# Kernel tuning notes

Measured on AMD Instinct MI355X. Metric: run time of the kernel, lower is better.

## Reference

```python
import jax, jax.numpy as jnp
import numpy as np

N_SRC = 50000      # columns of adj / rows of x
N_SAMP = 50000     # rows of adj (sampled nodes this layer)
N_TOTAL = 200000   # rows of historical embedding buffer
E = 1600000        # nnz of adj
D_IN = 256
D_OUT = 256


def setup_inputs() -> dict:
    key = jax.random.key(0)
    ks = jax.random.split(key, 10)
    x = jax.random.normal(ks[0], (N_SRC, D_IN), dtype=jnp.float32)
    adj_row = jax.random.randint(ks[1], (E,), 0, N_SAMP, dtype=jnp.int32)
    adj_col = jax.random.randint(ks[2], (E,), 0, N_SRC, dtype=jnp.int32)
    adj_val = jax.random.uniform(ks[3], (E,), dtype=jnp.float32)
    nodes_per_layer = jax.random.randint(ks[4], (N_SAMP,), 0, N_TOTAL, dtype=jnp.int32)
    y_buf = jax.random.normal(ks[5], (N_TOTAL, D_IN), dtype=jnp.float32)
    W = jax.random.normal(ks[6], (D_IN, D_OUT), dtype=jnp.float32) / np.sqrt(D_IN)
    b = jax.random.normal(ks[7], (D_OUT,), dtype=jnp.float32) * 0.01
    scale = jnp.ones((D_OUT,), dtype=jnp.float32)
    offset = jnp.zeros((D_OUT,), dtype=jnp.float32)
    return {"x": x, "adj_row": adj_row, "adj_col": adj_col, "adj_val": adj_val,
            "nodes_per_layer": nodes_per_layer, "y_buf": y_buf,
            "W": W, "b": b, "scale": scale, "offset": offset}


def reference(x, adj_row, adj_col, adj_val, nodes_per_layer, y_buf, W, b, scale, offset):
    # ---- sparse aggregation: feat = spmm(adj, x)  [N_SAMP, D_IN]
    msgs = adj_val[:, None] * x[adj_col]                         # [E, D_IN]
    feat = jax.ops.segment_sum(msgs, adj_row, num_segments=N_SAMP)
    # ---- momentum blend with historical embeddings (training path)
    feat = 0.9 * y_buf[nodes_per_layer] + 0.1 * feat
    # buffer update: sampled rows <- feat.detach(); all other rows *= 0.9
    new_y = (y_buf * 0.9).at[nodes_per_layer].set(jax.lax.stop_gradient(feat))
    # ---- linear -> ELU -> custom per-row normalization
    out = jax.nn.elu(feat @ W + b)                               # [N_SAMP, D_OUT]
    mean = out.mean(axis=1, keepdims=True)
    var = out.var(axis=1, keepdims=True) + 1e-9                  # unbiased=False
    out = (out - mean) * scale * jax.lax.rsqrt(var) + offset
    return out, new_y
```

## Files before the change

kernel.cpp:

```cpp
#include <hip/hip_runtime.h>
#include <hip/hip_fp16.h>
#include <math.h>

#define N_SRC   50000
#define N_SAMP  50000
#define N_TOTAL 200000
#define NE      1600000
#define D       256

#define CBSHIFT 11
#define NB      25
#define NCELL   (N_SAMP * NB)

typedef unsigned short ushort;
typedef unsigned int   uint;
using bf16x8 = __attribute__((ext_vector_type(8))) short;
using f32x4v = __attribute__((ext_vector_type(4))) float;

__device__ __forceinline__ float4 ntload4(const float* p) {
    f32x4v t = __builtin_nontemporal_load((const f32x4v*)p);
    return make_float4(t.x, t.y, t.z, t.w);
}
__device__ __forceinline__ void ntstore4(float* p, float4 v) {
    f32x4v t; t.x = v.x; t.y = v.y; t.z = v.z; t.w = v.w;
    __builtin_nontemporal_store(t, (f32x4v*)p);
}

__device__ __forceinline__ ushort bf16_rne(float f) {
    uint u = __float_as_uint(f);
    uint r = u + 0x7FFFu + ((u >> 16) & 1u);
    return (ushort)(r >> 16);
}
__device__ __forceinline__ float bf16_tof(ushort h) {
    return __uint_as_float(((uint)h) << 16);
}

__device__ __forceinline__ float4 xload4h(const __half* p) {
    int2 r = *(const int2*)p;
    __half2 h0 = *(__half2*)&r.x;
    __half2 h1 = *(__half2*)&r.y;
    float2 f0 = __half22float2(h0);
    float2 f1 = __half22float2(h1);
    return make_float4(f0.x, f0.y, f1.x, f1.y);
}

__device__ __forceinline__ void eunpack(uint e, int& col, float& val) {
    col = (int)(e & 0xFFFFu);
    val = __half2float(__ushort_as_half((ushort)(e >> 16)));
}

__global__ __launch_bounds__(256) void k_setup(
    int* __restrict__ cellcnt, int* __restrict__ owner, int* __restrict__ gtotal,
    const float* __restrict__ x, __half* __restrict__ xh,
    const float* __restrict__ W, ushort* __restrict__ Wt_hi, ushort* __restrict__ Wt_lo)
{
    int i = blockIdx.x * 256 + threadIdx.x;
    if (i < NCELL)   cellcnt[i] = 0;
    if (i < N_TOTAL) owner[i]   = -1;
    if (i == 0)      *gtotal    = 0;
    if (i < (N_SRC * D) / 8) {
        float4 a = ntload4(x + (size_t)i * 8);
        float4 c = ntload4(x + (size_t)i * 8 + 4);
        __half2 h0 = __floats2half2_rn(a.x, a.y);
        __half2 h1 = __floats2half2_rn(a.z, a.w);
        __half2 h2 = __floats2half2_rn(c.x, c.y);
        __half2 h3 = __floats2half2_rn(c.z, c.w);
        int4 w;
        w.x = *(int*)&h0; w.y = *(int*)&h1; w.z = *(int*)&h2; w.w = *(int*)&h3;
        *(int4*)(xh + (size_t)i * 8) = w;
    }
    if (i < D * D) {
        int k = i >> 8;
        int n = i & 255;
        float f = W[i];
        ushort h = bf16_rne(f);
        ushort l = bf16_rne(f - bf16_tof(h));
        Wt_hi[n * D + k] = h;
        Wt_lo[n * D + k] = l;
    }
}

__global__ __launch_bounds__(256) void k_count(
    const int* __restrict__ adj_row, const int* __restrict__ adj_col,
    const int* __restrict__ nodes, int* __restrict__ cellcnt, int* __restrict__ owner)
{
    int idx = blockIdx.x * 256 + threadIdx.x;
    if (idx < NE) {
        int row = __builtin_nontemporal_load(adj_row + idx);
        int col = __builtin_nontemporal_load(adj_col + idx);
        atomicAdd(&cellcnt[row * NB + (col >> CBSHIFT)], 1);
    }
    if (idx < N_SAMP) {
        atomicMax(&owner[nodes[idx]], idx);
    }
}

__global__ __launch_bounds__(256) void k_rowalloc(
    const int* __restrict__ cellcnt, int* __restrict__ cellcur,
    int* __restrict__ rowptr, int* __restrict__ rowcnt, int* __restrict__ gtotal)
{
    int r = blockIdx.x * 256 + threadIdx.x;
    if (r >= N_SAMP) return;
    int pref[NB];
    int sum = 0;
    #pragma unroll
    for (int cb = 0; cb < NB; ++cb) {
        pref[cb] = sum;
        sum += cellcnt[r * NB + cb];
    }
    int base = atomicAdd(gtotal, (sum + 3) & ~3);
    rowptr[r] = base;
    rowcnt[r] = sum;
    #pragma unroll
    for (int cb = 0; cb < NB; ++cb)
        cellcur[r * NB + cb] = base + pref[cb];
}

__global__ __launch_bounds__(256) void k_scatter(
    const int* __restrict__ adj_row, const int* __restrict__ adj_col,
    const float* __restrict__ adj_val, int* __restrict__ cellcur, uint* __restrict__ bucket)
{
    int idx = blockIdx.x * 256 + threadIdx.x;
    if (idx >= NE) return;
    int   row = __builtin_nontemporal_load(adj_row + idx);
    int   col = __builtin_nontemporal_load(adj_col + idx);
    float val = __builtin_nontemporal_load(adj_val + idx);
    uint  e   = (uint)col | ((uint)__half_as_ushort(__float2half_rn(val)) << 16);
    int pos = atomicAdd(&cellcur[row * NB + (col >> CBSHIFT)], 1);
    bucket[pos] = e;
}

__global__ __launch_bounds__(256) void k_spmm_blend(
    const __half* __restrict__ xh, const uint* __restrict__ bucket,
    const int* __restrict__ rowptr, const int* __restrict__ rowcnt,
    const int* __restrict__ nodes, const int* __restrict__ owner,
    const float* __restrict__ y_buf, float* __restrict__ feat, float* __restrict__ newy)
{
    int wave = threadIdx.x >> 6;
    int lane = threadIdx.x & 63;
    int row  = blockIdx.x * 4 + wave;
    int off  = lane * 4;

    int cnt = rowcnt[row];
    const uint* bk = bucket + rowptr[row];
    float4 acc = make_float4(0.f, 0.f, 0.f, 0.f);
    int j = 0;
    for (; j + 3 < cnt; j += 4) {
        uint4 ev = *(const uint4*)(bk + j);
        int c0, c1, c2, c3; float v0, v1, v2, v3;
        eunpack(ev.x, c0, v0); eunpack(ev.y, c1, v1);
        eunpack(ev.z, c2, v2); eunpack(ev.w, c3, v3);
        float4 x0 = xload4h(xh + (size_t)c0 * D + off);
        float4 x1 = xload4h(xh + (size_t)c1 * D + off);
        float4 x2 = xload4h(xh + (size_t)c2 * D + off);
        float4 x3 = xload4h(xh + (size_t)c3 * D + off);
        acc.x += v0 * x0.x + v1 * x1.x + v2 * x2.x + v3 * x3.x;
        acc.y += v0 * x0.y + v1 * x1.y + v2 * x2.y + v3 * x3.y;
        acc.z += v0 * x0.z + v1 * x1.z + v2 * x2.z + v3 * x3.z;
        acc.w += v0 * x0.w + v1 * x1.w + v2 * x2.w + v3 * x3.w;
    }
    for (; j < cnt; ++j) {
        int c0; float v0;
        eunpack(bk[j], c0, v0);
        float4 x0 = xload4h(xh + (size_t)c0 * D + off);
        acc.x += v0 * x0.x; acc.y += v0 * x0.y;
        acc.z += v0 * x0.z; acc.w += v0 * x0.w;
    }
    int node = nodes[row];
    float4 yv = *(const float4*)(y_buf + (size_t)node * D + off);
    float4 f;
    f.x = 0.9f * yv.x + 0.1f * acc.x;
    f.y = 0.9f * yv.y + 0.1f * acc.y;
    f.z = 0.9f * yv.z + 0.1f * acc.z;
    f.w = 0.9f * yv.w + 0.1f * acc.w;
    *(float4*)(feat + (size_t)row * D + off) = f;
    if (owner[node] == row)
        ntstore4(newy + (size_t)node * D + off, f);

    int base = row * 4;
    int4 ow = *(const int4*)&owner[base];
    #pragma unroll
    for (int k = 0; k < 4; ++k) {
        int o = (k == 0) ? ow.x : (k == 1) ? ow.y : (k == 2) ? ow.z : ow.w;
        if (o < 0) {
            int r = base + k;
            float4 y = *(const float4*)(y_buf + (size_t)r * D + off);
            ntstore4(newy + (size_t)r * D + off,
                     make_float4(0.9f * y.x, 0.9f * y.y, 0.9f * y.z, 0.9f * y.w));
        }
    }
}

__global__ __launch_bounds__(256) void k_gemm_elu_norm(
    float* __restrict__ io, const ushort* __restrict__ Wt_hi,
    const ushort* __restrict__ Wt_lo, const float* __restrict__ b,
    const float* __restrict__ scale, const float* __restrict__ offset)
{
    __shared__ ushort Fhi[32][264], Flo[32][264];
    __shared__ ushort Wh[256][40],  Wl[256][40];
    __shared__ float  red[2][2][16][2];

    int tid  = threadIdx.x;
    int w    = tid >> 6;
    int l    = tid & 63;
    int g    = l >> 4;
    int c16  = l & 15;
    int mt   = w & 1;
    int nh   = w >> 1;
    int r0   = blockIdx.x * 32;

    {
        int m  = tid >> 3;
        int c0 = (tid & 7) * 32;
        int r  = r0 + m;
        #pragma unroll
        for (int i = 0; i < 8; ++i) {
            float4 v = (r < N_SAMP) ? *(const float4*)(io + (size_t)r * D + c0 + i * 4)
                                    : make_float4(0.f, 0.f, 0.f, 0.f);
            ushort h0 = bf16_rne(v.x), h1 = bf16_rne(v.y);
            ushort h2 = bf16_rne(v.z), h3 = bf16_rne(v.w);
            ushort l0 = bf16_rne(v.x - bf16_tof(h0));
            ushort l1 = bf16_rne(v.y - bf16_tof(h1));
            ushort l2 = bf16_rne(v.z - bf16_tof(h2));
            ushort l3 = bf16_rne(v.w - bf16_tof(h3));
            int c = c0 + i * 4;
            uint2 ph, pl;
            ph.x = (uint)h0 | ((uint)h1 << 16); ph.y = (uint)h2 | ((uint)h3 << 16);
            pl.x = (uint)l0 | ((uint)l1 << 16); pl.y = (uint)l2 | ((uint)l3 << 16);
            *(uint2*)&Fhi[m][c] = ph;
            *(uint2*)&Flo[m][c] = pl;
        }
    }

    f32x4v acc[8];
    #pragma unroll
    for (int t = 0; t < 8; ++t) acc[t] = (f32x4v)(0.f);

    for (int kt8 = 0; kt8 < 8; ++kt8) {
        int kt = kt8 * 32;
        __syncthreads();
        {
            int n = tid;
            const int4* gh = (const int4*)(Wt_hi + (size_t)n * D + kt);
            const int4* gl = (const int4*)(Wt_lo + (size_t)n * D + kt);
            #pragma unroll
            for (int i = 0; i < 4; ++i) {
                *(int4*)&Wh[n][i * 8] = gh[i];
                *(int4*)&Wl[n][i * 8] = gl[i];
            }
        }
        __syncthreads();
        int arow = mt * 16 + c16;
        bf16x8 ah = *(const bf16x8*)&Fhi[arow][kt + g * 8];
        bf16x8 al = *(const bf16x8*)&Flo[arow][kt + g * 8];
        #pragma unroll
        for (int t = 0; t < 8; ++t) {
            int n = nh * 128 + t * 16 + c16;
            bf16x8 bh = *(const bf16x8*)&Wh[n][g * 8];
            bf16x8 bl = *(const bf16x8*)&Wl[n][g * 8];
            acc[t] = __builtin_amdgcn_mfma_f32_16x16x32_bf16(ah, bh, acc[t], 0, 0, 0);
            acc[t] = __builtin_amdgcn_mfma_f32_16x16x32_bf16(al, bh, acc[t], 0, 0, 0);
            acc[t] = __builtin_amdgcn_mfma_f32_16x16x32_bf16(ah, bl, acc[t], 0, 0, 0);
        }
    }

    float bcol[8], scol[8], ocol[8];
    #pragma unroll
    for (int t = 0; t < 8; ++t) {
        int c = nh * 128 + t * 16 + c16;
        bcol[t] = b[c]; scol[t] = scale[c]; ocol[t] = offset[c];
    }
    float s[4] = {0.f, 0.f, 0.f, 0.f};
    float q[4] = {0.f, 0.f, 0.f, 0.f};
    #pragma unroll
    for (int t = 0; t < 8; ++t) {
        #pragma unroll
        for (int j = 0; j < 4; ++j) {
            float o = acc[t][j] + bcol[t];
            o = o > 0.f ? o : expf(o) - 1.f;
            acc[t][j] = o;
            s[j] += o;
            q[j] += o * o;
        }
    }
    #pragma unroll
    for (int j = 0; j < 4; ++j) {
        #pragma unroll
        for (int d2 = 1; d2 < 16; d2 <<= 1) {
            s[j] += __shfl_xor(s[j], d2, 64);
            q[j] += __shfl_xor(q[j], d2, 64);
        }
    }
    if (c16 == 0) {
        #pragma unroll
        for (int j = 0; j < 4; ++j) {
            red[mt][nh][g * 4 + j][0] = s[j];
            red[mt][nh][g * 4 + j][1] = q[j];
        }
    }
    __syncthreads();
    #pragma unroll
    for (int j = 0; j < 4; ++j) {
        int rr = g * 4 + j;
        float S = red[mt][0][rr][0] + red[mt][1][rr][0];
        float Q = red[mt][0][rr][1] + red[mt][1][rr][1];
        float mean = S * (1.0f / 256.0f);
        float var  = Q * (1.0f / 256.0f) - mean * mean + 1e-9f;
        float rstd = rsqrtf(var);
        int r = r0 + mt * 16 + rr;
        if (r < N_SAMP) {
            #pragma unroll
            for (int t = 0; t < 8; ++t) {
                int c = nh * 128 + t * 16 + c16;
                io[(size_t)r * D + c] = (acc[t][j] - mean) * scol[t] * rstd + ocol[t];
            }
        }
    }
}

extern "C" void kernel_launch(void* const* d_in, const int* in_sizes, int n_in,
                              void* d_out, int out_size, void* d_ws, size_t ws_size,
                              hipStream_t stream) {
    const float* x       = (const float*)d_in[0];
    const int*   adj_row = (const int*)  d_in[1];
    const int*   adj_col = (const int*)  d_in[2];
    const float* adj_val = (const float*)d_in[3];
    const int*   nodes   = (const int*)  d_in[4];
    const float* y_buf   = (const float*)d_in[5];
    const float* Wm      = (const float*)d_in[6];
    const float* b       = (const float*)d_in[7];
    const float* scale   = (const float*)d_in[8];
    const float* offset  = (const float*)d_in[9];

    float* out  = (float*)d_out;
    float* newy = out + (size_t)N_SAMP * D;

    char*   ws      = (char*)d_ws;
    int*    cellcnt = (int*)(ws);
    int*    cellcur = (int*)(ws + 5  * 1024 * 1024);
    int*    rowptr  = (int*)(ws + 10 * 1024 * 1024);
    int*    rowcnt  = (int*)(ws + 10 * 1024 * 1024 + 256 * 1024);
    int*    gtotal  = (int*)(ws + 10 * 1024 * 1024 + 512 * 1024);
    int*    owner   = (int*)(ws + 11 * 1024 * 1024);
    ushort* Wt_hi   = (ushort*)(ws + 12 * 1024 * 1024);
    ushort* Wt_lo   = (ushort*)(ws + 12 * 1024 * 1024 + 128 * 1024);
    uint*   bucket  = (uint*)(ws + 13 * 1024 * 1024);
    __half* xh      = (__half*)(ws + 20 * 1024 * 1024);

    int setup_threads = (N_SRC * D) / 8;
    k_setup   <<<(setup_threads + 255) / 256, 256, 0, stream>>>(
        cellcnt, owner, gtotal, x, xh, Wm, Wt_hi, Wt_lo);
    k_count   <<<(NE + 255) / 256,     256, 0, stream>>>(adj_row, adj_col, nodes, cellcnt, owner);
    k_rowalloc<<<(N_SAMP + 255) / 256, 256, 0, stream>>>(cellcnt, cellcur, rowptr, rowcnt, gtotal);
    k_scatter <<<(NE + 255) / 256,     256, 0, stream>>>(adj_row, adj_col, adj_val, cellcur, bucket);
    k_spmm_blend<<<N_SAMP / 4, 256, 0, stream>>>(
        xh, bucket, rowptr, rowcnt, nodes, owner, y_buf, out, newy);
    k_gemm_elu_norm<<<(N_SAMP + 31) / 32, 256, 0, stream>>>(out, Wt_hi, Wt_lo, b, scale, offset);
}
```

Before: 786.9 us.

## Fuse CSR build kernels into one cooperative kernel, widen spmm unroll, coarser column buckets

Merges the setup, count, row-alloc and scatter kernels into one cooperative kernel with grid-wide syncs, which removes three launches and the gaps between them. Column buckets become coarser (13 instead of 25 per row), which shrinks the cell arrays. The SpMM inner loop is unrolled to 8 gathers per iteration to keep more loads in flight, and y_buf reads become nontemporal. The costs are grid-sync overhead, a fixed 1024-block grid that must be co-resident, and more register pressure in the SpMM loop.

```diff
diff --git a/kernel.cpp b/kernel.cpp
--- a/kernel.cpp
+++ b/kernel.cpp
@@ -1,6 +1,9 @@
 #include <hip/hip_runtime.h>
 #include <hip/hip_fp16.h>
+#include <hip/hip_cooperative_groups.h>
 #include <math.h>
+
+namespace cg = cooperative_groups;
 
 #define N_SRC   50000
 #define N_SAMP  50000
@@ -8,8 +11,8 @@
 #define NE      1600000
 #define D       256
 
-#define CBSHIFT 11
-#define NB      25
+#define CBSHIFT 12
+#define NB      13
 #define NCELL   (N_SAMP * NB)
 
 typedef unsigned short ushort;
@@ -49,16 +52,23 @@
     val = __half2float(__ushort_as_half((ushort)(e >> 16)));
 }
 
-__global__ __launch_bounds__(256) void k_setup(
-    int* __restrict__ cellcnt, int* __restrict__ owner, int* __restrict__ gtotal,
+__global__ __launch_bounds__(256, 4) void k_build(
     const float* __restrict__ x, __half* __restrict__ xh,
-    const float* __restrict__ W, ushort* __restrict__ Wt_hi, ushort* __restrict__ Wt_lo)
+    const float* __restrict__ W, ushort* __restrict__ Wt_hi, ushort* __restrict__ Wt_lo,
+    const int* __restrict__ adj_row, const int* __restrict__ adj_col,
+    const float* __restrict__ adj_val, const int* __restrict__ nodes,
+    int* __restrict__ cellcnt, int* __restrict__ cellcur,
+    int* __restrict__ rowptr, int* __restrict__ rowcnt,
+    int* __restrict__ gtotal, int* __restrict__ owner, uint* __restrict__ bucket)
 {
-    int i = blockIdx.x * 256 + threadIdx.x;
-    if (i < NCELL)   cellcnt[i] = 0;
-    if (i < N_TOTAL) owner[i]   = -1;
-    if (i == 0)      *gtotal    = 0;
-    if (i < (N_SRC * D) / 8) {
+    cg::grid_group grid = cg::this_grid();
+    int tid = blockIdx.x * 256 + threadIdx.x;
+    int nth = gridDim.x * 256;
+
+    for (int i = tid; i < NCELL; i += nth) cellcnt[i] = 0;
+    for (int i = tid; i < N_TOTAL; i += nth) owner[i] = -1;
+    if (tid == 0) *gtotal = 0;
+    for (int i = tid; i < (N_SRC * D) / 8; i += nth) {
         float4 a = ntload4(x + (size_t)i * 8);
         float4 c = ntload4(x + (size_t)i * 8 + 4);
         __half2 h0 = __floats2half2_rn(a.x, a.y);
@@ -69,7 +79,7 @@
         w.x = *(int*)&h0; w.y = *(int*)&h1; w.z = *(int*)&h2; w.w = *(int*)&h3;
         *(int4*)(xh + (size_t)i * 8) = w;
     }
-    if (i < D * D) {
+    for (int i = tid; i < D * D; i += nth) {
         int k = i >> 8;
         int n = i & 255;
         float f = W[i];
@@ -78,56 +88,43 @@
         Wt_hi[n * D + k] = h;
         Wt_lo[n * D + k] = l;
     }
-}
-
-__global__ __launch_bounds__(256) void k_count(
-    const int* __restrict__ adj_row, const int* __restrict__ adj_col,
-    const int* __restrict__ nodes, int* __restrict__ cellcnt, int* __restrict__ owner)
-{
-    int idx = blockIdx.x * 256 + threadIdx.x;
-    if (idx < NE) {
-        int row = __builtin_nontemporal_load(adj_row + idx);
-        int col = __builtin_nontemporal_load(adj_col + idx);
+    grid.sync();
+
+    for (int i = tid; i < NE; i += nth) {
+        int row = __builtin_nontemporal_load(adj_row + i);
+        int col = __builtin_nontemporal_load(adj_col + i);
         atomicAdd(&cellcnt[row * NB + (col >> CBSHIFT)], 1);
     }
-    if (idx < N_SAMP) {
-        atomicMax(&owner[nodes[idx]], idx);
-    }
-}
-
-__global__ __launch_bounds__(256) void k_rowalloc(
-    const int* __restrict__ cellcnt, int* __restrict__ cellcur,
-    int* __restrict__ rowptr, int* __restrict__ rowcnt, int* __restrict__ gtotal)
-{
-    int r = blockIdx.x * 256 + threadIdx.x;
-    if (r >= N_SAMP) return;
-    int pref[NB];
-    int sum = 0;
-    #pragma unroll
-    for (int cb = 0; cb < NB; ++cb) {
-        pref[cb] = sum;
-        sum += cellcnt[r * NB + cb];
-    }
-    int base = atomicAdd(gtotal, (sum + 3) & ~3);
-    rowptr[r] = base;
-    rowcnt[r] = sum;
-    #pragma unroll
-    for (int cb = 0; cb < NB; ++cb)
-        cellcur[r * NB + cb] = base + pref[cb];
-}
-
-__global__ __launch_bounds__(256) void k_scatter(
-    const int* __restrict__ adj_row, const int* __restrict__ adj_col,
-    const float* __restrict__ adj_val, int* __restrict__ cellcur, uint* __restrict__ bucket)
-{
-    int idx = blockIdx.x * 256 + threadIdx.x;
-    if (idx >= NE) return;
-    int   row = __builtin_nontemporal_load(adj_row + idx);
-    int   col = __builtin_nontemporal_load(adj_col + idx);
-    float val = __builtin_nontemporal_load(adj_val + idx);
-    uint  e   = (uint)col | ((uint)__half_as_ushort(__float2half_rn(val)) << 16);
-    int pos = atomicAdd(&cellcur[row * NB + (col >> CBSHIFT)], 1);
-    bucket[pos] = e;
+    for (int i = tid; i < N_SAMP; i += nth) {
+        atomicMax(&owner[nodes[i]], i);
+    }
+    grid.sync();
+
+    for (int r = tid; r < N_SAMP; r += nth) {
+        int pref[NB];
+        int sum = 0;
+        #pragma unroll
+        for (int cb = 0; cb < NB; ++cb) {
+            pref[cb] = sum;
+            sum += cellcnt[r * NB + cb];
+        }
+        int base = atomicAdd(gtotal, (sum + 3) & ~3);
+        rowptr[r] = base;
+        rowcnt[r] = sum;
+        #pragma unroll
+        for (int cb = 0; cb < NB; ++cb)
+            cellcur[r * NB + cb] = base + pref[cb];
+    }
+    grid.sync();
+
+    for (int i = tid; i < NE; i += nth) {
+        int   row = __builtin_nontemporal_load(adj_row + i);
+        int   col = __builtin_nontemporal_load(adj_col + i);
+        float val = __builtin_nontemporal_load(adj_val + i);
+        uint  e   = (uint)col | ((uint)__half_as_ushort(__float2half_rn(val)) << 16);
+        int pos = atomicAdd(&cellcur[row * NB + (col >> CBSHIFT)], 1);
+        bucket[pos] = e;
+    }
 }
 
 __global__ __launch_bounds__(256) void k_spmm_blend(
@@ -145,19 +142,31 @@
     const uint* bk = bucket + rowptr[row];
     float4 acc = make_float4(0.f, 0.f, 0.f, 0.f);
     int j = 0;
-    for (; j + 3 < cnt; j += 4) {
-        uint4 ev = *(const uint4*)(bk + j);
-        int c0, c1, c2, c3; float v0, v1, v2, v3;
-        eunpack(ev.x, c0, v0); eunpack(ev.y, c1, v1);
-        eunpack(ev.z, c2, v2); eunpack(ev.w, c3, v3);
+    for (; j + 7 < cnt; j += 8) {
+        uint4 ea = *(const uint4*)(bk + j);
+        uint4 eb = *(const uint4*)(bk + j + 4);
+        int c0, c1, c2, c3, c4, c5, c6, c7;
+        float v0, v1, v2, v3, v4, v5, v6, v7;
+        eunpack(ea.x, c0, v0); eunpack(ea.y, c1, v1);
+        eunpack(ea.z, c2, v2); eunpack(ea.w, c3, v3);
+        eunpack(eb.x, c4, v4); eunpack(eb.y, c5, v5);
+        eunpack(eb.z, c6, v6); eunpack(eb.w, c7, v7);
         float4 x0 = xload4h(xh + (size_t)c0 * D + off);
         float4 x1 = xload4h(xh + (size_t)c1 * D + off);
         float4 x2 = xload4h(xh + (size_t)c2 * D + off);
         float4 x3 = xload4h(xh + (size_t)c3 * D + off);
-        acc.x += v0 * x0.x + v1 * x1.x + v2 * x2.x + v3 * x3.x;
-        acc.y += v0 * x0.y + v1 * x1.y + v2 * x2.y + v3 * x3.y;
-        acc.z += v0 * x0.z + v1 * x1.z + v2 * x2.z + v3 * x3.z;
-        acc.w += v0 * x0.w + v1 * x1.w + v2 * x2.w + v3 * x3.w;
+        float4 x4 = xload4h(xh + (size_t)c4 * D + off);
+        float4 x5 = xload4h(xh + (size_t)c5 * D + off);
+        float4 x6 = xload4h(xh + (size_t)c6 * D + off);
+        float4 x7 = xload4h(xh + (size_t)c7 * D + off);
+        acc.x += v0 * x0.x + v1 * x1.x + v2 * x2.x + v3 * x3.x
+               + v4 * x4.x + v5 * x5.x + v6 * x6.x + v7 * x7.x;
+        acc.y += v0 * x0.y + v1 * x1.y + v2 * x2.y + v3 * x3.y
+               + v4 * x4.y + v5 * x5.y + v6 * x6.y + v7 * x7.y;
+        acc.z += v0 * x0.z + v1 * x1.z + v2 * x2.z + v3 * x3.z
+               + v4 * x4.z + v5 * x5.z + v6 * x6.z + v7 * x7.z;
+        acc.w += v0 * x0.w + v1 * x1.w + v2 * x2.w + v3 * x3.w
+               + v4 * x4.w + v5 * x5.w + v6 * x6.w + v7 * x7.w;
     }
     for (; j < cnt; ++j) {
         int c0; float v0;
@@ -167,7 +176,7 @@
         acc.z += v0 * x0.z; acc.w += v0 * x0.w;
     }
     int node = nodes[row];
-    float4 yv = *(const float4*)(y_buf + (size_t)node * D + off);
+    float4 yv = ntload4(y_buf + (size_t)node * D + off);
     float4 f;
     f.x = 0.9f * yv.x + 0.1f * acc.x;
     f.y = 0.9f * yv.y + 0.1f * acc.y;
@@ -184,7 +193,7 @@
         int o = (k == 0) ? ow.x : (k == 1) ? ow.y : (k == 2) ? ow.z : ow.w;
         if (o < 0) {
             int r = base + k;
-            float4 y = *(const float4*)(y_buf + (size_t)r * D + off);
+            float4 y = ntload4(y_buf + (size_t)r * D + off);
             ntstore4(newy + (size_t)r * D + off,
                      make_float4(0.9f * y.x, 0.9f * y.y, 0.9f * y.z, 0.9f * y.w));
         }
@@ -337,22 +346,23 @@
 
     char*   ws      = (char*)d_ws;
     int*    cellcnt = (int*)(ws);
-    int*    cellcur = (int*)(ws + 5  * 1024 * 1024);
-    int*    rowptr  = (int*)(ws + 10 * 1024 * 1024);
-    int*    rowcnt  = (int*)(ws + 10 * 1024 * 1024 + 256 * 1024);
-    int*    gtotal  = (int*)(ws + 10 * 1024 * 1024 + 512 * 1024);
-    int*    owner   = (int*)(ws + 11 * 1024 * 1024);
-    ushort* Wt_hi   = (ushort*)(ws + 12 * 1024 * 1024);
-    ushort* Wt_lo   = (ushort*)(ws + 12 * 1024 * 1024 + 128 * 1024);
-    uint*   bucket  = (uint*)(ws + 13 * 1024 * 1024);
-    __half* xh      = (__half*)(ws + 20 * 1024 * 1024);
-
-    int setup_threads = (N_SRC * D) / 8;
-    k_setup   <<<(setup_threads + 255) / 256, 256, 0, stream>>>(
-        cellcnt, owner, gtotal, x, xh, Wm, Wt_hi, Wt_lo);
-    k_count   <<<(NE + 255) / 256,     256, 0, stream>>>(adj_row, adj_col, nodes, cellcnt, owner);
-    k_rowalloc<<<(N_SAMP + 255) / 256, 256, 0, stream>>>(cellcnt, cellcur, rowptr, rowcnt, gtotal);
-    k_scatter <<<(NE + 255) / 256,     256, 0, stream>>>(adj_row, adj_col, adj_val, cellcur, bucket);
+    int*    cellcur = (int*)(ws + 3 * 1024 * 1024);
+    int*    rowptr  = (int*)(ws + 6 * 1024 * 1024);
+    int*    rowcnt  = (int*)(ws + 6 * 1024 * 1024 + 256 * 1024);
+    int*    gtotal  = (int*)(ws + 6 * 1024 * 1024 + 512 * 1024);
+    int*    owner   = (int*)(ws + 7 * 1024 * 1024);
+    ushort* Wt_hi   = (ushort*)(ws + 8 * 1024 * 1024);
+    ushort* Wt_lo   = (ushort*)(ws + 8 * 1024 * 1024 + 256 * 1024);
+    uint*   bucket  = (uint*)(ws + 9 * 1024 * 1024);
+    __half* xh      = (__half*)(ws + 17 * 1024 * 1024);
+
+    void* bargs[] = {
+        (void*)&x, (void*)&xh, (void*)&Wm, (void*)&Wt_hi, (void*)&Wt_lo,
+        (void*)&adj_row, (void*)&adj_col, (void*)&adj_val, (void*)&nodes,
+        (void*)&cellcnt, (void*)&cellcur, (void*)&rowptr, (void*)&rowcnt,
+        (void*)&gtotal, (void*)&owner, (void*)&bucket};
+    hipLaunchCooperativeKernel(k_build, dim3(1024), dim3(256), bargs, 0u, stream);
+
     k_spmm_blend<<<N_SAMP / 4, 256, 0, stream>>>(
         xh, bucket, rowptr, rowcnt, nodes, owner, y_buf, out, newy);
     k_gemm_elu_norm<<<(N_SAMP + 31) / 32, 256, 0, stream>>>(out, Wt_hi, Wt_lo, b, scale, offset);
```

Measured after the change: 1.119 ms. 1.42x slower.
